# Kernel optimization log

Measured on AMD Instinct MI355X. Metric: run time of the kernel, lower is better.

Reference implementation:

```python
import jax, jax.numpy as jnp
import numpy as np

SEQ_LEN = 96
PRED_LEN = 16
HIDDEN = 64
FEAT = 7
BATCH = 512


def setup_inputs() -> dict:
    key = jax.random.key(0)
    ks = jax.random.split(key, 7)
    s = 1.0 / np.sqrt(HIDDEN)  # PyTorch LSTM/Linear default uniform init bound
    x = jax.random.normal(ks[0], (BATCH, SEQ_LEN, FEAT), jnp.float32)
    W_ih = jax.random.uniform(ks[1], (4 * HIDDEN, FEAT), jnp.float32, -s, s)
    W_hh = jax.random.uniform(ks[2], (4 * HIDDEN, HIDDEN), jnp.float32, -s, s)
    b_ih = jax.random.uniform(ks[3], (4 * HIDDEN,), jnp.float32, -s, s)
    b_hh = jax.random.uniform(ks[4], (4 * HIDDEN,), jnp.float32, -s, s)
    fc_W = jax.random.uniform(ks[5], (FEAT, HIDDEN), jnp.float32, -s, s)
    fc_b = jax.random.uniform(ks[6], (FEAT,), jnp.float32, -s, s)
    return {"x": x, "W_ih": W_ih, "W_hh": W_hh, "b_ih": b_ih, "b_hh": b_hh,
            "fc_W": fc_W, "fc_b": fc_b}


def _lstm_last(x, h, c, W_ih, W_hh, b):
    # Precompute input-to-gate projections for the whole window: [B, T, 4H]
    xg = jnp.einsum('bti,gi->btg', x, W_ih) + b

    def cell(carry, xg_t):
        h, c = carry
        gates = xg_t + h @ W_hh.T            # [B, 4H], PyTorch gate order i,f,g,o
        i, f, g, o = jnp.split(gates, 4, axis=-1)
        i = jax.nn.sigmoid(i)
        f = jax.nn.sigmoid(f)
        g = jnp.tanh(g)
        o = jax.nn.sigmoid(o)
        c = f * c + i * g
        h = o * jnp.tanh(c)
        return (h, c), None

    (h, c), _ = jax.lax.scan(cell, (h, c), jnp.swapaxes(xg, 0, 1))
    return h, c


def reference(x, W_ih, W_hh, b_ih, b_hh, fc_W, fc_b):
    B = x.shape[0]
    b = b_ih + b_hh
    h = jnp.zeros((B, HIDDEN), x.dtype)
    c = jnp.zeros((B, HIDDEN), x.dtype)
    outs = []
    for _ in range(PRED_LEN):
        h, c = _lstm_last(x, h, c, W_ih, W_hh, b)
        pred = h @ fc_W.T + fc_b             # [B, 7]
        outs.append(pred)
        x = jnp.concatenate([x[:, 1:, :], pred[:, None, :]], axis=1)
    return jnp.stack(outs, axis=1)           # [B, PRED_LEN, 7]
```

## Files before the change

### kernel.cpp

```cpp
#include <hip/hip_runtime.h>

#define SEQ_LEN 96
#define PRED_LEN 16
#define HIDDEN 64
#define FEAT 7
#define BATCH 512
#define TL (SEQ_LEN + PRED_LEN)
#define XSTR 8

typedef float v2f __attribute__((ext_vector_type(2)));

#define L2E 1.4426950408889634f

__device__ __forceinline__ float qp_xor1(float v) {
    return __int_as_float(__builtin_amdgcn_mov_dpp(__float_as_int(v), 0xB1, 0xF, 0xF, true));
}

__global__ __launch_bounds__(128)
__attribute__((amdgpu_waves_per_eu(1, 1)))
__attribute__((amdgpu_num_vgpr(256)))
void lstm_ar_kernel(
    const float* __restrict__ x,
    const float* __restrict__ W_ih,
    const float* __restrict__ W_hh,
    const float* __restrict__ b_ih,
    const float* __restrict__ b_hh,
    const float* __restrict__ fc_W,
    const float* __restrict__ fc_b,
    float* __restrict__ out)
{
    __shared__ float xs[TL * XSTR];
    __shared__ float hb0[HIDDEN];
    __shared__ float hb1[HIDDEN];
    __shared__ float fcw[FEAT * HIDDEN];
    __shared__ float fcb[FEAT];

    const int tid = threadIdx.x;
    const int b   = blockIdx.x;
    const int u   = tid >> 1;
    const int s   = tid & 1;

    v2f wh[4][16];
    #pragma unroll
    for (int g = 0; g < 4; ++g) {
        const float* wr = W_hh + (u + (g << 6)) * HIDDEN + (s << 5);
        #pragma unroll
        for (int j = 0; j < 16; ++j) wh[g][j] = *(const v2f*)(wr + 2 * j);
    }
    v2f wx[4][2];
    #pragma unroll
    for (int g = 0; g < 4; ++g)
        #pragma unroll
        for (int i = 0; i < 2; ++i) {
            int c0 = (s << 2) + 2 * i, c1 = c0 + 1;
            wx[g][i].x = W_ih[(u + (g << 6)) * FEAT + c0];
            wx[g][i].y = (c1 < FEAT) ? W_ih[(u + (g << 6)) * FEAT + c1] : 0.0f;
        }
    float bias[4];
    #pragma unroll
    for (int g = 0; g < 4; ++g)
        bias[g] = (s == 0) ? (b_ih[u + (g << 6)] + b_hh[u + (g << 6)]) : 0.0f;

    const float bk  = (s == 1) ? (-2.0f * L2E) : (-L2E);
    const float bm  = (s == 1) ? 2.0f : 1.0f;
    const float bbc = (s == 1) ? -1.0f : 0.0f;

    for (int i = tid; i < TL * XSTR; i += 128) {
        int row = i >> 3, f = i & 7;
        float v = 0.0f;
        if (row < SEQ_LEN && f < FEAT) v = x[b * SEQ_LEN * FEAT + row * FEAT + f];
        xs[i] = v;
    }
    for (int i = tid; i < FEAT * HIDDEN; i += 128) fcw[i] = fc_W[i];
    if (tid < FEAT)   fcb[tid] = fc_b[tid];
    if (tid < HIDDEN) hb0[tid] = 0.0f;
    float c = 0.0f;
    __syncthreads();

    auto step = [&](float4 xv, int nrow,
                    const float* __restrict__ hr, float* __restrict__ hw) -> float4 {
        const float4* h4 = (const float4*)(hr + (s << 5));

        v2f A0, A1, A2, A3;
        A0.x = bias[0]; A0.y = 0.0f;
        A1.x = bias[1]; A1.y = 0.0f;
        A2.x = bias[2]; A2.y = 0.0f;
        A3.x = bias[3]; A3.y = 0.0f;
        v2f xlo; xlo.x = xv.x; xlo.y = xv.y;
        v2f xhi; xhi.x = xv.z; xhi.y = xv.w;
        A0 = __builtin_elementwise_fma(wx[0][0], xlo, A0);
        A1 = __builtin_elementwise_fma(wx[1][0], xlo, A1);
        A2 = __builtin_elementwise_fma(wx[2][0], xlo, A2);
        A3 = __builtin_elementwise_fma(wx[3][0], xlo, A3);
        A0 = __builtin_elementwise_fma(wx[0][1], xhi, A0);
        A1 = __builtin_elementwise_fma(wx[1][1], xhi, A1);
        A2 = __builtin_elementwise_fma(wx[2][1], xhi, A2);
        A3 = __builtin_elementwise_fma(wx[3][1], xhi, A3);

        #pragma unroll
        for (int j = 0; j < 8; ++j) {
            float4 hv = h4[j];
            v2f hlo; hlo.x = hv.x; hlo.y = hv.y;
            v2f hhi; hhi.x = hv.z; hhi.y = hv.w;
            A0 = __builtin_elementwise_fma(wh[0][2*j],   hlo, A0);
            A1 = __builtin_elementwise_fma(wh[1][2*j],   hlo, A1);
            A2 = __builtin_elementwise_fma(wh[2][2*j],   hlo, A2);
            A3 = __builtin_elementwise_fma(wh[3][2*j],   hlo, A3);
            A0 = __builtin_elementwise_fma(wh[0][2*j+1], hhi, A0);
            A1 = __builtin_elementwise_fma(wh[1][2*j+1], hhi, A1);
            A2 = __builtin_elementwise_fma(wh[2][2*j+1], hhi, A2);
            A3 = __builtin_elementwise_fma(wh[3][2*j+1], hhi, A3);
        }

        float r0 = A0.x + A0.y, r1 = A1.x + A1.y;
        float r2 = A2.x + A2.y, r3 = A3.x + A3.y;
        r0 += qp_xor1(r0); r1 += qp_xor1(r1);
        r2 += qp_xor1(r2); r3 += qp_xor1(r3);

        float aa = s ? r0 : r1;
        float ab = s ? r2 : r3;
        float ea = __builtin_amdgcn_exp2f(aa * (-L2E));
        float va = __builtin_amdgcn_rcpf(1.0f + ea);
        float eb = __builtin_amdgcn_exp2f(ab * bk);
        float rb = __builtin_amdgcn_rcpf(1.0f + eb);
        float vb = fmaf(bm, rb, bbc);

        float pa = qp_xor1(va);
        float pb = qp_xor1(vb);
        float gi = s ? va : pa;
        float gf = s ? pa : va;
        float gg = s ? vb : pb;
        float go = s ? pb : vb;

        c = fmaf(gf, c, gi * gg);
        float e2 = __builtin_amdgcn_exp2f(c * (-2.0f * L2E));
        float rr = __builtin_amdgcn_rcpf(1.0f + e2);
        float th = fmaf(2.0f, rr, -1.0f);
        float h  = go * th;

        hw[u] = h;

        float4 nxt = *(const float4*)&xs[nrow * XSTR + (s << 2)];
        __syncthreads();
        return nxt;
    };

    for (int k = 0; k < PRED_LEN; ++k) {
        float4 xv = *(const float4*)&xs[k * XSTR + (s << 2)];
        for (int t = 0; t < SEQ_LEN; t += 2) {
            xv = step(xv, k + t + 1, hb0, hb1);
            xv = step(xv, k + t + 2, hb1, hb0);
        }

        if (tid < FEAT) {
            float p0 = fcb[tid], p1 = 0.0f, p2 = 0.0f, p3 = 0.0f;
            const float4* hh = (const float4*)hb0;
            #pragma unroll
            for (int j = 0; j < 16; ++j) {
                float4 hv = hh[j];
                p0 = fmaf(fcw[tid * HIDDEN + 4*j + 0], hv.x, p0);
                p1 = fmaf(fcw[tid * HIDDEN + 4*j + 1], hv.y, p1);
                p2 = fmaf(fcw[tid * HIDDEN + 4*j + 2], hv.z, p2);
                p3 = fmaf(fcw[tid * HIDDEN + 4*j + 3], hv.w, p3);
            }
            float pred = (p0 + p1) + (p2 + p3);
            out[(b * PRED_LEN + k) * FEAT + tid] = pred;
            xs[(SEQ_LEN + k) * XSTR + tid] = pred;
        }
        __syncthreads();
    }
}

extern "C" void kernel_launch(void* const* d_in, const int* in_sizes, int n_in,
                              void* d_out, int out_size, void* d_ws, size_t ws_size,
                              hipStream_t stream) {
    const float* x    = (const float*)d_in[0];
    const float* W_ih = (const float*)d_in[1];
    const float* W_hh = (const float*)d_in[2];
    const float* b_ih = (const float*)d_in[3];
    const float* b_hh = (const float*)d_in[4];
    const float* fc_W = (const float*)d_in[5];
    const float* fc_b = (const float*)d_in[6];
    float* out = (float*)d_out;

    lstm_ar_kernel<<<BATCH, 128, 0, stream>>>(x, W_ih, W_hh, b_ih, b_hh, fc_W, fc_b, out);
}
```

Baseline: 539.7 us.

## Precompute input-gate projections into an fp16 LDS table outside the recurrence

Computes W_ih·x plus the bias for all 96 window rows once per block and stores the result in shared memory as fp16, pre-split by 0.5 so both half-lanes add one share. Each predicted output's projection is appended after the step. This removes the per-step input FMAs and bias setup from the serial recurrent path, and the per-step load shrinks to 8 bytes. The cost is extra LDS capacity and a setup pass. Storing gate pre-activations in half precision may cost accuracy. The explicit VGPR cap attribute is also dropped.

```diff
diff --git a/kernel.cpp b/kernel.cpp
--- a/kernel.cpp
+++ b/kernel.cpp
@@ -6,9 +6,9 @@
 #define FEAT 7
 #define BATCH 512
 #define TL (SEQ_LEN + PRED_LEN)
-#define XSTR 8
-
-typedef float v2f __attribute__((ext_vector_type(2)));
+
+typedef float    v2f __attribute__((ext_vector_type(2)));
+typedef _Float16 v4h __attribute__((ext_vector_type(4)));
 
 #define L2E 1.4426950408889634f
 
@@ -18,7 +18,6 @@
 
 __global__ __launch_bounds__(128)
 __attribute__((amdgpu_waves_per_eu(1, 1)))
-__attribute__((amdgpu_num_vgpr(256)))
 void lstm_ar_kernel(
     const float* __restrict__ x,
     const float* __restrict__ W_ih,
@@ -29,11 +28,15 @@
     const float* __restrict__ fc_b,
     float* __restrict__ out)
 {
-    __shared__ float xs[TL * XSTR];
+    __shared__ __align__(16) _Float16 xg[TL * HIDDEN * 4];
     __shared__ float hb0[HIDDEN];
     __shared__ float hb1[HIDDEN];
+    __shared__ float wihs[256 * FEAT];
+    __shared__ float bias256[256];
     __shared__ float fcw[FEAT * HIDDEN];
     __shared__ float fcb[FEAT];
+    __shared__ float predbuf[8];
+    __shared__ float xtmp[SEQ_LEN * 8];
 
     const int tid = threadIdx.x;
     const int b   = blockIdx.x;
@@ -47,56 +50,54 @@
         #pragma unroll
         for (int j = 0; j < 16; ++j) wh[g][j] = *(const v2f*)(wr + 2 * j);
     }
-    v2f wx[4][2];
-    #pragma unroll
-    for (int g = 0; g < 4; ++g)
-        #pragma unroll
-        for (int i = 0; i < 2; ++i) {
-            int c0 = (s << 2) + 2 * i, c1 = c0 + 1;
-            wx[g][i].x = W_ih[(u + (g << 6)) * FEAT + c0];
-            wx[g][i].y = (c1 < FEAT) ? W_ih[(u + (g << 6)) * FEAT + c1] : 0.0f;
-        }
-    float bias[4];
-    #pragma unroll
-    for (int g = 0; g < 4; ++g)
-        bias[g] = (s == 0) ? (b_ih[u + (g << 6)] + b_hh[u + (g << 6)]) : 0.0f;
 
     const float bk  = (s == 1) ? (-2.0f * L2E) : (-L2E);
     const float bm  = (s == 1) ? 2.0f : 1.0f;
     const float bbc = (s == 1) ? -1.0f : 0.0f;
 
-    for (int i = tid; i < TL * XSTR; i += 128) {
+    for (int i = tid; i < SEQ_LEN * 8; i += 128) {
         int row = i >> 3, f = i & 7;
-        float v = 0.0f;
-        if (row < SEQ_LEN && f < FEAT) v = x[b * SEQ_LEN * FEAT + row * FEAT + f];
-        xs[i] = v;
-    }
+        xtmp[i] = (f < FEAT) ? x[b * SEQ_LEN * FEAT + row * FEAT + f] : 0.0f;
+    }
+    for (int i = tid; i < 256 * FEAT; i += 128) wihs[i] = W_ih[i];
+    for (int i = tid; i < 256; i += 128) bias256[i] = b_ih[i] + b_hh[i];
     for (int i = tid; i < FEAT * HIDDEN; i += 128) fcw[i] = fc_W[i];
     if (tid < FEAT)   fcb[tid] = fc_b[tid];
     if (tid < HIDDEN) hb0[tid] = 0.0f;
+    __syncthreads();
+
+    #pragma unroll
+    for (int e = 0; e < 2; ++e) {
+        const int grow = tid + (e << 7);
+        const int uu = grow & 63, gg = grow >> 6;
+        float w0 = wihs[grow * FEAT + 0], w1 = wihs[grow * FEAT + 1];
+        float w2 = wihs[grow * FEAT + 2], w3 = wihs[grow * FEAT + 3];
+        float w4 = wihs[grow * FEAT + 4], w5 = wihs[grow * FEAT + 5];
+        float w6 = wihs[grow * FEAT + 6];
+        const float bb = bias256[grow];
+        for (int row = 0; row < SEQ_LEN; ++row) {
+            float4 xa = *(const float4*)&xtmp[row * 8];
+            float4 xbv = *(const float4*)&xtmp[row * 8 + 4];
+            float acc = bb;
+            acc = fmaf(w0, xa.x, acc);
+            acc = fmaf(w1, xa.y, acc);
+            acc = fmaf(w2, xa.z, acc);
+            acc = fmaf(w3, xa.w, acc);
+            acc = fmaf(w4, xbv.x, acc);
+            acc = fmaf(w5, xbv.y, acc);
+            acc = fmaf(w6, xbv.z, acc);
+            xg[(row * HIDDEN + uu) * 4 + gg] = (_Float16)(0.5f * acc);
+        }
+    }
+    __syncthreads();
+
     float c = 0.0f;
-    __syncthreads();
-
-    auto step = [&](float4 xv, int nrow,
-                    const float* __restrict__ hr, float* __restrict__ hw) -> float4 {
+
+    auto step = [&](v4h xgv, int nrow,
+                    const float* __restrict__ hr, float* __restrict__ hw) -> v4h {
         const float4* h4 = (const float4*)(hr + (s << 5));
 
-        v2f A0, A1, A2, A3;
-        A0.x = bias[0]; A0.y = 0.0f;
-        A1.x = bias[1]; A1.y = 0.0f;
-        A2.x = bias[2]; A2.y = 0.0f;
-        A3.x = bias[3]; A3.y = 0.0f;
-        v2f xlo; xlo.x = xv.x; xlo.y = xv.y;
-        v2f xhi; xhi.x = xv.z; xhi.y = xv.w;
-        A0 = __builtin_elementwise_fma(wx[0][0], xlo, A0);
-        A1 = __builtin_elementwise_fma(wx[1][0], xlo, A1);
-        A2 = __builtin_elementwise_fma(wx[2][0], xlo, A2);
-        A3 = __builtin_elementwise_fma(wx[3][0], xlo, A3);
-        A0 = __builtin_elementwise_fma(wx[0][1], xhi, A0);
-        A1 = __builtin_elementwise_fma(wx[1][1], xhi, A1);
-        A2 = __builtin_elementwise_fma(wx[2][1], xhi, A2);
-        A3 = __builtin_elementwise_fma(wx[3][1], xhi, A3);
-
+        v2f A0 = {0.0f, 0.0f}, A1 = A0, A2 = A0, A3 = A0;
         #pragma unroll
         for (int j = 0; j < 8; ++j) {
             float4 hv = h4[j];
@@ -112,8 +113,10 @@
             A3 = __builtin_elementwise_fma(wh[3][2*j+1], hhi, A3);
         }
 
-        float r0 = A0.x + A0.y, r1 = A1.x + A1.y;
-        float r2 = A2.x + A2.y, r3 = A3.x + A3.y;
+        float r0 = (A0.x + A0.y) + (float)xgv[0];
+        float r1 = (A1.x + A1.y) + (float)xgv[1];
+        float r2 = (A2.x + A2.y) + (float)xgv[2];
+        float r3 = (A3.x + A3.y) + (float)xgv[3];
         r0 += qp_xor1(r0); r1 += qp_xor1(r1);
         r2 += qp_xor1(r2); r3 += qp_xor1(r3);
 
@@ -140,13 +143,13 @@
 
         hw[u] = h;
 
-        float4 nxt = *(const float4*)&xs[nrow * XSTR + (s << 2)];
+        v4h nxt = *(const v4h*)&xg[(nrow * HIDDEN + u) * 4];
         __syncthreads();
         return nxt;
     };
 
     for (int k = 0; k < PRED_LEN; ++k) {
-        float4 xv = *(const float4*)&xs[k * XSTR + (s << 2)];
+        v4h xv = *(const v4h*)&xg[(k * HIDDEN + u) * 4];
         for (int t = 0; t < SEQ_LEN; t += 2) {
             xv = step(xv, k + t + 1, hb0, hb1);
             xv = step(xv, k + t + 2, hb1, hb0);
@@ -165,7 +168,19 @@
             }
             float pred = (p0 + p1) + (p2 + p3);
             out[(b * PRED_LEN + k) * FEAT + tid] = pred;
-            xs[(SEQ_LEN + k) * XSTR + tid] = pred;
+            predbuf[tid] = pred;
+        }
+        __syncthreads();
+
+        #pragma unroll
+        for (int e = 0; e < 2; ++e) {
+            const int grow = tid + (e << 7);
+            float acc = bias256[grow];
+            #pragma unroll
+            for (int f = 0; f < FEAT; ++f)
+                acc = fmaf(wihs[grow * FEAT + f], predbuf[f], acc);
+            xg[((SEQ_LEN + k) * HIDDEN + (grow & 63)) * 4 + (grow >> 6)] =
+                (_Float16)(0.5f * acc);
         }
         __syncthreads();
     }
```

New measurement: 572.3 us. 1.06x slower.
